# Performance work log

Measured on AMD Instinct MI355X. Metric: run time of the kernel, lower is better.

Reference implementation:

```python
import jax, jax.numpy as jnp
import numpy as np

EPS = 1e-6
H, HKV, D = 32, 8, 64          # heads, kv heads, head_dim
E, TOP_K, FF = 8, 2, 1024      # experts, top-k, expert intermediate
HID = 2048


def rms_norm(x, w):
    xf = x.astype(jnp.float32)
    var = jnp.mean(xf * xf, axis=-1, keepdims=True)
    return (w * (xf * jax.lax.rsqrt(var + EPS)).astype(x.dtype))


def rotate_half(x):
    x1, x2 = jnp.split(x, 2, axis=-1)
    return jnp.concatenate([-x2, x1], axis=-1)


def apply_rope(q, k, cos, sin):
    # cos/sin: [B,S,rd] -> [B,1,S,rd]
    cos = cos[:, None, :, :]
    sin = sin[:, None, :, :]
    rd = cos.shape[-1]
    q_rot, q_pass = q[..., :rd], q[..., rd:]
    k_rot, k_pass = k[..., :rd], k[..., rd:]
    q_emb = q_rot * cos + rotate_half(q_rot) * sin
    k_emb = k_rot * cos + rotate_half(k_rot) * sin
    return (jnp.concatenate([q_emb, q_pass], -1), jnp.concatenate([k_emb, k_pass], -1))


def attention(x, cos, sin, wq, wk, wv, wo):
    B, S, _ = x.shape
    q = (x @ wq).reshape(B, S, H, D).transpose(0, 2, 1, 3)      # [B,H,S,D]
    k = (x @ wk).reshape(B, S, HKV, D).transpose(0, 2, 1, 3)    # [B,Hk,S,D]
    v = (x @ wv).reshape(B, S, HKV, D).transpose(0, 2, 1, 3)
    q, k = apply_rope(q, k, cos, sin)
    rep = H // HKV
    k = jnp.repeat(k, rep, axis=1)
    v = jnp.repeat(v, rep, axis=1)
    scale = D ** -0.5
    scores = jnp.einsum('bhqd,bhkd->bhqk', q, k) * scale
    causal = jnp.triu(jnp.full((S, S), -jnp.inf, dtype=scores.dtype), k=1)
    scores = scores + causal
    probs = jax.nn.softmax(scores.astype(jnp.float32), axis=-1).astype(q.dtype)
    out = jnp.einsum('bhqk,bhkd->bhqd', probs, v)
    out = out.transpose(0, 2, 1, 3).reshape(B, S, H * D)
    return out @ wo


def moe(x, gate_w, corr_bias, w1, w2, w3):
    B, S, Dm = x.shape
    xf = x.reshape(-1, Dm)                                      # [T, Dm]
    T = xf.shape[0]
    logits = xf @ gate_w                                        # [T, E]
    rw = jax.nn.sigmoid(logits.astype(jnp.float32))
    scores = rw + corr_bias
    _, sel = jax.lax.top_k(scores, TOP_K)                       # [T, k]
    tw = jnp.take_along_axis(rw, sel, axis=-1)
    tw = tw / jnp.sum(tw, axis=-1, keepdims=True)
    # dense [T, E] combine weights (zero for unselected experts)
    cw = jnp.zeros((T, E), dtype=xf.dtype).at[jnp.arange(T)[:, None], sel].set(tw.astype(xf.dtype))
    # run every expert densely, combine with sparse weights (same math as gather/scatter loop)
    h = jax.nn.silu(jnp.einsum('td,edf->etf', xf, w1)) * jnp.einsum('td,edf->etf', xf, w3)
    eo = jnp.einsum('etf,efd->etd', h, w2)                      # [E, T, Dm]
    out = jnp.einsum('etd,te->td', eo, cw)
    return out.reshape(B, S, Dm)


def setup_inputs() -> dict:
    key = jax.random.key(0)
    ks = jax.random.split(key, 16)
    s = 0.02
    return {
        'hidden_states': jax.random.normal(ks[0], (2, 1024, HID), jnp.float32),
        'cos': jax.random.uniform(ks[1], (2, 1024, D), jnp.float32),
        'sin': jax.random.uniform(ks[2], (2, 1024, D), jnp.float32),
        'ln1_w': jnp.ones((HID,), jnp.float32),
        'ln2_w': jnp.ones((HID,), jnp.float32),
        'wq': jax.random.normal(ks[3], (HID, H * D), jnp.float32) * s,
        'wk': jax.random.normal(ks[4], (HID, HKV * D), jnp.float32) * s,
        'wv': jax.random.normal(ks[5], (HID, HKV * D), jnp.float32) * s,
        'wo': jax.random.normal(ks[6], (H * D, HID), jnp.float32) * s,
        'gate_w': jax.random.normal(ks[7], (HID, E), jnp.float32) * s,
        'corr_bias': jnp.zeros((E,), jnp.float32),
        'w1': jax.random.normal(ks[8], (E, HID, FF), jnp.float32) * s,
        'w2': jax.random.normal(ks[9], (E, FF, HID), jnp.float32) * s,
        'w3': jax.random.normal(ks[10], (E, HID, FF), jnp.float32) * s,
    }


def reference(hidden_states, cos, sin, ln1_w, ln2_w, wq, wk, wv, wo, gate_w, corr_bias, w1, w2, w3):
    residual = hidden_states
    h = rms_norm(hidden_states, ln1_w)
    h = attention(h, cos, sin, wq, wk, wv, wo)
    h = residual + h
    residual = h
    h = rms_norm(h, ln2_w)
    h = moe(h, gate_w, corr_bias, w1, w2, w3)
    return residual + h
```

## Files before the change

### kernel.cpp

```cpp
#include <hip/hip_runtime.h>
#include <hip/hip_bf16.h>

#define DEV static __device__ __forceinline__

typedef __attribute__((ext_vector_type(8))) short short8;
typedef __attribute__((ext_vector_type(8))) __bf16 bf16x8;
typedef __attribute__((ext_vector_type(4))) float floatx4;

DEV short f2bf(float f) {
  unsigned u = __builtin_bit_cast(unsigned, f);
  unsigned r = (u + 0x7fffu + ((u >> 16) & 1u)) >> 16;
  return (short)(unsigned short)r;
}
DEV float bf2f(short s) {
  unsigned u = ((unsigned)(unsigned short)s) << 16;
  return __builtin_bit_cast(float, u);
}
DEV floatx4 mfma16(short8 a, short8 b, floatx4 c) {
  return __builtin_amdgcn_mfma_f32_16x16x32_bf16(
      __builtin_bit_cast(bf16x8, a), __builtin_bit_cast(bf16x8, b), c, 0, 0, 0);
}

DEV int sw2(int r) { return (r ^ (r >> 2)) & 3; }

DEV const short* sbase(const short* src, int ld, int row0, int id) {
  int r = id >> 2, cc = id & 3;
  return src + (long)(row0 + r) * ld + ((cc ^ sw2(r)) << 3);
}
DEV const short* sbaseg(const short* src, int ld, const int* rows, int p0, int plim,
                        int id) {
  int r = id >> 2, cc = id & 3;
  int pi = p0 + r;
  if (pi > plim) pi = plim;
  return src + (long)rows[pi] * ld + ((cc ^ sw2(r)) << 3);
}
DEV void sissue(short* ldsbuf, const short* base, int k0, int tid, int slotbase) {
  int wave = tid >> 6;
  __builtin_amdgcn_global_load_lds(
      (const __attribute__((address_space(1))) void*)(base + k0),
      (__attribute__((address_space(3))) void*)(ldsbuf + (slotbase + wave * 64) * 8),
      16, 0, 0);
}
DEV short8 rdfrag(const short* lds, int row, int l4) {
  return *(const short8*)(lds + row * 32 + ((l4 ^ sw2(row)) << 3));
}

__global__ __launch_bounds__(256) void k_gemm_qkv(
    const short* Ah, const short* Al, const short* Bh, const short* Bl,
    short* qbh, short* qbl, short* kbh, short* kbl, short* vbh, short* vbl,
    const float* cs, const float* sn) {
  const int K = 2048;
  __shared__ __align__(16) short AsH[2][4096], AsL[2][4096], BsH[2][2048], BsL[2][2048];
  int tid = threadIdx.x, lane = tid & 63, wave = tid >> 6;
  int l15 = lane & 15, l4 = lane >> 4;
  int m0 = blockIdx.y * 128, n0 = blockIdx.x * 64;

  const short* bAH0 = sbase(Ah, K, m0, tid);
  const short* bAH1 = sbase(Ah, K, m0, tid + 256);
  const short* bAL0 = sbase(Al, K, m0, tid);
  const short* bAL1 = sbase(Al, K, m0, tid + 256);
  const short* bBH0 = sbase(Bh, K, n0, tid);
  const short* bBL0 = sbase(Bl, K, n0, tid);

  auto STAGE = [&](int buf, int k0) {
    sissue(AsH[buf], bAH0, k0, tid, 0);
    sissue(AsH[buf], bAH1, k0, tid, 256);
    sissue(AsL[buf], bAL0, k0, tid, 0);
    sissue(AsL[buf], bAL1, k0, tid, 256);
    sissue(BsH[buf], bBH0, k0, tid, 0);
    sissue(BsL[buf], bBL0, k0, tid, 0);
  };

  floatx4 zero4 = {0.f, 0.f, 0.f, 0.f};
  floatx4 acc[2][4];
#pragma unroll
  for (int i = 0; i < 2; ++i)
#pragma unroll
    for (int j = 0; j < 4; ++j) acc[i][j] = zero4;

  STAGE(0, 0);
  __syncthreads();
  int cur = 0;
  for (int k0 = 0; k0 < K; k0 += 32) {
    if (k0 + 32 < K) STAGE(cur ^ 1, k0 + 32);
    short8 ah[2], al[2], bh2[4], bl2[4];
#pragma unroll
    for (int mi = 0; mi < 2; ++mi) {
      ah[mi] = rdfrag(AsH[cur], wave * 32 + mi * 16 + l15, l4);
      al[mi] = rdfrag(AsL[cur], wave * 32 + mi * 16 + l15, l4);
    }
#pragma unroll
    for (int nt = 0; nt < 4; ++nt) {
      bh2[nt] = rdfrag(BsH[cur], nt * 16 + l15, l4);
      bl2[nt] = rdfrag(BsL[cur], nt * 16 + l15, l4);
    }
#pragma unroll
    for (int mi = 0; mi < 2; ++mi)
#pragma unroll
      for (int nt = 0; nt < 4; ++nt) {
        acc[mi][nt] = mfma16(al[mi], bh2[nt], acc[mi][nt]);
        acc[mi][nt] = mfma16(ah[mi], bl2[nt], acc[mi][nt]);
        acc[mi][nt] = mfma16(ah[mi], bh2[nt], acc[mi][nt]);
      }
    __syncthreads();
    cur ^= 1;
  }

  bool isq = n0 < 2048, isk = (!isq) && n0 < 2560;
  if (isq || isk) {
#pragma unroll
    for (int mi = 0; mi < 2; ++mi)
#pragma unroll
      for (int ntp = 0; ntp < 2; ++ntp)
#pragma unroll
        for (int j = 0; j < 4; ++j) {
          int row = m0 + wave * 32 + mi * 16 + l4 * 4 + j;
          int d = ntp * 16 + l15;
          float x0 = acc[mi][ntp][j], x1 = acc[mi][ntp + 2][j];
          float c0 = cs[row * 64 + d], c1 = cs[row * 64 + d + 32];
          float s0 = sn[row * 64 + d], s1 = sn[row * 64 + d + 32];
          float y0 = x0 * c0 - x1 * s0;
          float y1 = x1 * c1 + x0 * s1;
          if (isq) { y0 *= 0.125f; y1 *= 0.125f; }
          acc[mi][ntp][j] = y0;
          acc[mi][ntp + 2][j] = y1;
        }
  }
  short* Ch; short* Cl; int ldc, coff;
  if (isq)      { Ch = qbh; Cl = qbl; ldc = 2048; coff = n0; }
  else if (isk) { Ch = kbh; Cl = kbl; ldc = 512;  coff = n0 - 2048; }
  else          { Ch = vbh; Cl = vbl; ldc = 512;  coff = n0 - 2560; }
#pragma unroll
  for (int mi = 0; mi < 2; ++mi)
#pragma unroll
    for (int nt = 0; nt < 4; ++nt) {
      int row = m0 + wave * 32 + mi * 16 + l4 * 4;
      int col = coff + nt * 16 + l15;
#pragma unroll
      for (int j = 0; j < 4; ++j) {
        float v = acc[mi][nt][j];
        long ix = (long)(row + j) * ldc + col;
        short hi = f2bf(v);
        Ch[ix] = hi;
        Cl[ix] = f2bf(v - bf2f(hi));
      }
    }
}

__global__ __launch_bounds__(256) void k_gemm_wo(const short* Ah, const short* Al,
                                                 const short* Bh, const short* Bl,
                                                 const float* resid, float* out) {
  const int K = 2048;
  __shared__ __align__(16) short AsH[2][4096], AsL[2][4096], BsH[2][2048], BsL[2][2048];
  int tid = threadIdx.x, lane = tid & 63, wave = tid >> 6;
  int l15 = lane & 15, l4 = lane >> 4;
  int m0 = blockIdx.y * 128, n0 = blockIdx.x * 64;

  const short* bAH0 = sbase(Ah, K, m0, tid);
  const short* bAH1 = sbase(Ah, K, m0, tid + 256);
  const short* bAL0 = sbase(Al, K, m0, tid);
  const short* bAL1 = sbase(Al, K, m0, tid + 256);
  const short* bBH0 = sbase(Bh, K, n0, tid);
  const short* bBL0 = sbase(Bl, K, n0, tid);

  auto STAGE = [&](int buf, int k0) {
    sissue(AsH[buf], bAH0, k0, tid, 0);
    sissue(AsH[buf], bAH1, k0, tid, 256);
    sissue(AsL[buf], bAL0, k0, tid, 0);
    sissue(AsL[buf], bAL1, k0, tid, 256);
    sissue(BsH[buf], bBH0, k0, tid, 0);
    sissue(BsL[buf], bBL0, k0, tid, 0);
  };

  floatx4 zero4 = {0.f, 0.f, 0.f, 0.f};
  floatx4 acc[2][4];
#pragma unroll
  for (int i = 0; i < 2; ++i)
#pragma unroll
    for (int j = 0; j < 4; ++j) acc[i][j] = zero4;

  STAGE(0, 0);
  __syncthreads();
  int cur = 0;
  for (int k0 = 0; k0 < K; k0 += 32) {
    if (k0 + 32 < K) STAGE(cur ^ 1, k0 + 32);
    short8 ah[2], al[2], bh2[4], bl2[4];
#pragma unroll
    for (int mi = 0; mi < 2; ++mi) {
      ah[mi] = rdfrag(AsH[cur], wave * 32 + mi * 16 + l15, l4);
      al[mi] = rdfrag(AsL[cur], wave * 32 + mi * 16 + l15, l4);
    }
#pragma unroll
    for (int nt = 0; nt < 4; ++nt) {
      bh2[nt] = rdfrag(BsH[cur], nt * 16 + l15, l4);
      bl2[nt] = rdfrag(BsL[cur], nt * 16 + l15, l4);
    }
#pragma unroll
    for (int mi = 0; mi < 2; ++mi)
#pragma unroll
      for (int nt = 0; nt < 4; ++nt) {
        acc[mi][nt] = mfma16(al[mi], bh2[nt], acc[mi][nt]);
        acc[mi][nt] = mfma16(ah[mi], bl2[nt], acc[mi][nt]);
        acc[mi][nt] = mfma16(ah[mi], bh2[nt], acc[mi][nt]);
      }
    __syncthreads();
    cur ^= 1;
  }
#pragma unroll
  for (int mi = 0; mi < 2; ++mi)
#pragma unroll
    for (int nt = 0; nt < 4; ++nt) {
      int row = m0 + wave * 32 + mi * 16 + l4 * 4;
      int col = n0 + nt * 16 + l15;
#pragma unroll
      for (int j = 0; j < 4; ++j) {
        long ix = (long)(row + j) * 2048 + col;
        out[ix] = resid[ix] + acc[mi][nt][j];
      }
    }
}

__global__ __launch_bounds__(256) void k_moe_a(const short* X, const short* W1T,
                                               const short* W3T, const int* rows,
                                               const int* cnt, const int* eoff,
                                               short* hh) {
  int e = blockIdx.z;
  int c = cnt[e];
  int mtile = blockIdx.y;
  if (mtile * 128 >= c) return;
  int p0 = eoff[e] + mtile * 128;
  int plim = eoff[e] + c - 1;
  const short* B1 = W1T + (long)e * 1024 * 2048;
  const short* B3 = W3T + (long)e * 1024 * 2048;
  int n0 = blockIdx.x * 64;
  __shared__ __align__(16) short As_[2][4096], B1s[2][2048], B3s[2][2048];
  int tid = threadIdx.x, lane = tid & 63, wave = tid >> 6;
  int l15 = lane & 15, l4 = lane >> 4;

  const short* bA0 = sbaseg(X, 2048, rows, p0, plim, tid);
  const short* bA1 = sbaseg(X, 2048, rows, p0, plim, tid + 256);
  const short* bB1 = sbase(B1, 2048, n0, tid);
  const short* bB3 = sbase(B3, 2048, n0, tid);

  auto STAGE = [&](int buf, int k0) {
    sissue(As_[buf], bA0, k0, tid, 0);
    sissue(As_[buf], bA1, k0, tid, 256);
    sissue(B1s[buf], bB1, k0, tid, 0);
    sissue(B3s[buf], bB3, k0, tid, 0);
  };

  floatx4 zero4 = {0.f, 0.f, 0.f, 0.f};
  floatx4 acc1[2][4], acc3[2][4];
#pragma unroll
  for (int i = 0; i < 2; ++i)
#pragma unroll
    for (int j = 0; j < 4; ++j) { acc1[i][j] = zero4; acc3[i][j] = zero4; }

  STAGE(0, 0);
  __syncthreads();
  int cur = 0;
  for (int k0 = 0; k0 < 2048; k0 += 32) {
    if (k0 + 32 < 2048) STAGE(cur ^ 1, k0 + 32);
    short8 af[2], b1f[4], b3f[4];
#pragma unroll
    for (int mi = 0; mi < 2; ++mi) af[mi] = rdfrag(As_[cur], wave * 32 + mi * 16 + l15, l4);
#pragma unroll
    for (int nt = 0; nt < 4; ++nt) {
      b1f[nt] = rdfrag(B1s[cur], nt * 16 + l15, l4);
      b3f[nt] = rdfrag(B3s[cur], nt * 16 + l15, l4);
    }
#pragma unroll
    for (int mi = 0; mi < 2; ++mi)
#pragma unroll
      for (int nt = 0; nt < 4; ++nt) {
        acc1[mi][nt] = mfma16(af[mi], b1f[nt], acc1[mi][nt]);
        acc3[mi][nt] = mfma16(af[mi], b3f[nt], acc3[mi][nt]);
      }
    __syncthreads();
    cur ^= 1;
  }
#pragma unroll
  for (int mi = 0; mi < 2; ++mi)
#pragma unroll
    for (int nt = 0; nt < 4; ++nt) {
      int col = n0 + nt * 16 + l15;
#pragma unroll
      for (int j = 0; j < 4; ++j) {
        int rl = wave * 32 + mi * 16 + l4 * 4 + j;
        if (mtile * 128 + rl < c) {
          float v1 = acc1[mi][nt][j], v3 = acc3[mi][nt][j];
          float hg = v1 / (1.f + __expf(-v1));
          hh[(long)(p0 + rl) * 1024 + col] = f2bf(hg * v3);
        }
      }
    }
}

__global__ __launch_bounds__(256) void k_moe_b(const short* hh, const short* W2T,
                                               const int* cnt, const int* eoff,
                                               short* mo) {
  int e = blockIdx.z;
  int c = cnt[e];
  int mtile = blockIdx.y;
  if (mtile * 128 >= c) return;
  int p0 = eoff[e] + mtile * 128;
  const short* B = W2T + (long)e * 2048 * 1024;
  int n0 = blockIdx.x * 128;
  __shared__ __align__(16) short As_[2][4096], Bs_[2][4096];
  int tid = threadIdx.x, lane = tid & 63, wave = tid >> 6;
  int l15 = lane & 15, l4 = lane >> 4;
  int wm = wave >> 1, wn = wave & 1;

  const short* bA0 = sbase(hh, 1024, p0, tid);
  const short* bA1 = sbase(hh, 1024, p0, tid + 256);
  const short* bB0 = sbase(B, 1024, n0, tid);
  const short* bB1 = sbase(B, 1024, n0, tid + 256);

  auto STAGE = [&](int buf, int k0) {
    sissue(As_[buf], bA0, k0, tid, 0);
    sissue(As_[buf], bA1, k0, tid, 256);
    sissue(Bs_[buf], bB0, k0, tid, 0);
    sissue(Bs_[buf], bB1, k0, tid, 256);
  };

  floatx4 zero4 = {0.f, 0.f, 0.f, 0.f};
  floatx4 acc[4][4];
#pragma unroll
  for (int i = 0; i < 4; ++i)
#pragma unroll
    for (int j = 0; j < 4; ++j) acc[i][j] = zero4;

  STAGE(0, 0);
  __syncthreads();
  int cur = 0;
  for (int k0 = 0; k0 < 1024; k0 += 32) {
    if (k0 + 32 < 1024) STAGE(cur ^ 1, k0 + 32);
    short8 af[4], bfv[4];
#pragma unroll
    for (int mi = 0; mi < 4; ++mi) af[mi] = rdfrag(As_[cur], wm * 64 + mi * 16 + l15, l4);
#pragma unroll
    for (int nt = 0; nt < 4; ++nt) bfv[nt] = rdfrag(Bs_[cur], wn * 64 + nt * 16 + l15, l4);
#pragma unroll
    for (int mi = 0; mi < 4; ++mi)
#pragma unroll
      for (int nt = 0; nt < 4; ++nt) acc[mi][nt] = mfma16(af[mi], bfv[nt], acc[mi][nt]);
    __syncthreads();
    cur ^= 1;
  }
#pragma unroll
  for (int mi = 0; mi < 4; ++mi)
#pragma unroll
    for (int nt = 0; nt < 4; ++nt) {
      int col = n0 + wn * 64 + nt * 16 + l15;
#pragma unroll
      for (int j = 0; j < 4; ++j) {
        int rl = wm * 64 + mi * 16 + l4 * 4 + j;
        if (mtile * 128 + rl < c) mo[(long)(p0 + rl) * 2048 + col] = f2bf(acc[mi][nt][j]);
      }
    }
}

DEV int aswz(int r, int c) { return r * 64 + (((c ^ ((r ^ (r >> 3)) & 7)) & 7) << 3); }

__global__ __launch_bounds__(256) void k_attn2(const short* qhp, const short* qlp,
                                               const short* khp, const short* klp,
                                               const short* vhp, const short* vlp,
                                               short* oh, short* ol) {
  int qt = blockIdx.x, bh = blockIdx.y;
  int h = bh & 31, b = bh >> 5, kvh = h >> 2;
  int tid = threadIdx.x, wave = tid >> 6, lane = tid & 63;
  int l15 = lane & 15, l4 = lane >> 4;

  __shared__ __align__(16) short Kh[4096], Kl2[4096], Vth[4096], Vtl[4096];
  __shared__ __align__(16) short Ph[4][1024], Pl2[4][1024];

  int qrow = qt * 64 + wave * 16 + l15;
  long qoff = ((long)(b * 1024 + qrow)) * 2048 + h * 64;
  short8 qh0 = *(const short8*)(qhp + qoff + l4 * 8);
  short8 qh1 = *(const short8*)(qhp + qoff + 32 + l4 * 8);
  short8 ql0 = *(const short8*)(qlp + qoff + l4 * 8);
  short8 ql1 = *(const short8*)(qlp + qoff + 32 + l4 * 8);

  floatx4 zero4 = {0.f, 0.f, 0.f, 0.f};
  floatx4 acco[4] = {zero4, zero4, zero4, zero4};
  float mrun[4] = {-1e30f, -1e30f, -1e30f, -1e30f};
  float lrun[4] = {0.f, 0.f, 0.f, 0.f};

  const short* khb = khp + ((long)b * 1024) * 512 + kvh * 64;
  const short* klb = klp + ((long)b * 1024) * 512 + kvh * 64;
  const short* vhb = vhp + ((long)b * 1024) * 512 + kvh * 64;
  const short* vlb = vlp + ((long)b * 1024) * 512 + kvh * 64;

  for (int kt = 0; kt <= qt; ++kt) {
#pragma unroll
    for (int it = 0; it < 2; ++it) {
      int id = it * 256 + tid;
      int r = id >> 3, cc = id & 7;
      long goff = (long)(kt * 64 + r) * 512 + cc * 8;
      *(uint4*)(Kh + aswz(r, cc)) = *(const uint4*)(khb + goff);
      *(uint4*)(Kl2 + aswz(r, cc)) = *(const uint4*)(klb + goff);
      __align__(16) short tv[8];
      *(uint4*)tv = *(const uint4*)(vhb + goff);
#pragma unroll
      for (int j = 0; j < 8; ++j) Vth[aswz(cc * 8 + j, r >> 3) + (r & 7)] = tv[j];
      *(uint4*)tv = *(const uint4*)(vlb + goff);
#pragma unroll
      for (int j = 0; j < 8; ++j) Vtl[aswz(cc * 8 + j, r >> 3) + (r & 7)] = tv[j];
    }
    __syncthreads();

    floatx4 accs[4] = {zero4, zero4, zero4, zero4};
#pragma unroll
    for (int ks = 0; ks < 2; ++ks) {
      short8 qah = ks ? qh1 : qh0;
      short8 qal = ks ? ql1 : ql0;
#pragma unroll
      for (int nt = 0; nt < 4; ++nt) {
        int kvr = nt * 16 + l15;
        short8 kfh = *(const short8*)(Kh + aswz(kvr, l4 + 4 * ks));
        short8 kfl = *(const short8*)(Kl2 + aswz(kvr, l4 + 4 * ks));
        accs[nt] = mfma16(qal, kfh, accs[nt]);
        accs[nt] = mfma16(qah, kfl, accs[nt]);
        accs[nt] = mfma16(qah, kfh, accs[nt]);
      }
    }
    if (kt == qt) {
#pragma unroll
      for (int nt = 0; nt < 4; ++nt)
#pragma unroll
        for (int j = 0; j < 4; ++j) {
          int kvg = nt * 16 + l15;
          int qg = wave * 16 + l4 * 4 + j;
          if (kvg > qg) accs[nt][j] = -1e30f;
        }
    }
    float pj[4][4];
#pragma unroll
    for (int j = 0; j < 4; ++j) {
      float mx = fmaxf(fmaxf(accs[0][j], accs[1][j]), fmaxf(accs[2][j], accs[3][j]));
      mx = fmaxf(mx, __shfl_xor(mx, 1));
      mx = fmaxf(mx, __shfl_xor(mx, 2));
      mx = fmaxf(mx, __shfl_xor(mx, 4));
      mx = fmaxf(mx, __shfl_xor(mx, 8));
      float mnew = fmaxf(mrun[j], mx);
      float alpha = expf(mrun[j] - mnew);
      float rs = 0.f;
#pragma unroll
      for (int nt = 0; nt < 4; ++nt) {
        float pv = expf(accs[nt][j] - mnew);
        pj[nt][j] = pv;
        rs += pv;
      }
      rs += __shfl_xor(rs, 1);
      rs += __shfl_xor(rs, 2);
      rs += __shfl_xor(rs, 4);
      rs += __shfl_xor(rs, 8);
      lrun[j] = lrun[j] * alpha + rs;
      mrun[j] = mnew;
      acco[0][j] *= alpha; acco[1][j] *= alpha; acco[2][j] *= alpha; acco[3][j] *= alpha;
    }
    short* P = Ph[wave];
    short* P2 = Pl2[wave];
#pragma unroll
    for (int nt = 0; nt < 4; ++nt)
#pragma unroll
      for (int j = 0; j < 4; ++j) {
        int rr = l4 * 4 + j, col = nt * 16 + l15;
        float pv = pj[nt][j];
        short hi = f2bf(pv);
        int ad = aswz(rr, col >> 3) + (col & 7);
        P[ad] = hi;
        P2[ad] = f2bf(pv - bf2f(hi));
      }
    asm volatile("s_waitcnt lgkmcnt(0)" ::: "memory");
    __builtin_amdgcn_sched_barrier(0);
#pragma unroll
    for (int ks = 0; ks < 2; ++ks) {
      short8 pah = *(const short8*)(P + aswz(l15, l4 + 4 * ks));
      short8 pal = *(const short8*)(P2 + aswz(l15, l4 + 4 * ks));
#pragma unroll
      for (int nt = 0; nt < 4; ++nt) {
        int dr = nt * 16 + l15;
        short8 vfh = *(const short8*)(Vth + aswz(dr, l4 + 4 * ks));
        short8 vfl = *(const short8*)(Vtl + aswz(dr, l4 + 4 * ks));
        acco[nt] = mfma16(pal, vfh, acco[nt]);
        acco[nt] = mfma16(pah, vfl, acco[nt]);
        acco[nt] = mfma16(pah, vfh, acco[nt]);
      }
    }
    __syncthreads();
  }
#pragma unroll
  for (int j = 0; j < 4; ++j) {
    float invl = 1.f / lrun[j];
    int qg = qt * 64 + wave * 16 + l4 * 4 + j;
    long ooff = ((long)(b * 1024 + qg)) * 2048 + h * 64;
#pragma unroll
    for (int nt = 0; nt < 4; ++nt) {
      float v = acco[nt][j] * invl;
      short hi = f2bf(v);
      oh[ooff + nt * 16 + l15] = hi;
      ol[ooff + nt * 16 + l15] = f2bf(v - bf2f(hi));
    }
  }
}

DEV void trans_load(const float* src, int N, int n0, int k0, float (*t)[65], int tid) {
  int r = tid >> 2, cq = tid & 3;
  const float* s = src + (long)(k0 + r) * N + n0 + cq * 16;
#pragma unroll
  for (int i = 0; i < 4; ++i) {
    float4 v = *(const float4*)(s + i * 4);
    t[r][cq * 16 + i * 4 + 0] = v.x;
    t[r][cq * 16 + i * 4 + 1] = v.y;
    t[r][cq * 16 + i * 4 + 2] = v.z;
    t[r][cq * 16 + i * 4 + 3] = v.w;
  }
}

DEV void trans_tile1(const float* src, short* dst, int N, int K, int n0, int k0,
                     float (*t)[65]) {
  int tid = threadIdx.x;
  trans_load(src, N, n0, k0, t, tid);
  __syncthreads();
  int n = tid >> 2, kc = tid & 3;
#pragma unroll
  for (int ii = 0; ii < 2; ++ii) {
    short8 o;
#pragma unroll
    for (int j = 0; j < 8; ++j) o[j] = f2bf(t[kc * 16 + ii * 8 + j][n]);
    *(short8*)(dst + (long)(n0 + n) * K + k0 + kc * 16 + ii * 8) = o;
  }
}

DEV void trans_tile2(const float* src, short* dh, short* dl, int N, int K, int n0,
                     int k0, float (*t)[65]) {
  int tid = threadIdx.x;
  trans_load(src, N, n0, k0, t, tid);
  __syncthreads();
  int n = tid >> 2, kc = tid & 3;
#pragma unroll
  for (int ii = 0; ii < 2; ++ii) {
    short8 ohv, olv;
#pragma unroll
    for (int j = 0; j < 8; ++j) {
      float v = t[kc * 16 + ii * 8 + j][n];
      short hi = f2bf(v);
      ohv[j] = hi;
      olv[j] = f2bf(v - bf2f(hi));
    }
    *(short8*)(dh + (long)(n0 + n) * K + k0 + kc * 16 + ii * 8) = ohv;
    *(short8*)(dl + (long)(n0 + n) * K + k0 + kc * 16 + ii * 8) = olv;
  }
}

__global__ __launch_bounds__(256) void k_trans_attn(
    const float* wq, const float* wk, const float* wv, const float* wo,
    short* qkvTh, short* qkvTl, short* woTh, short* woTl) {
  __shared__ float t[64][65];
  int x = blockIdx.x, kt = blockIdx.y;
  const float* src; short* dh; short* dl; int N, n0;
  if (x < 32)      { src = wq; dh = qkvTh; dl = qkvTl; N = 2048; n0 = x * 64; }
  else if (x < 40) { src = wk; dh = qkvTh + 2048L * 2048; dl = qkvTl + 2048L * 2048;
                     N = 512; n0 = (x - 32) * 64; }
  else if (x < 48) { src = wv; dh = qkvTh + 2560L * 2048; dl = qkvTl + 2560L * 2048;
                     N = 512; n0 = (x - 40) * 64; }
  else             { src = wo; dh = woTh; dl = woTl; N = 2048; n0 = (x - 48) * 64; }
  trans_tile2(src, dh, dl, N, 2048, n0, kt * 64, t);
}

__global__ __launch_bounds__(256) void k_trans_moe13(const float* w1, const float* w3,
                                                     short* w1T, short* w3T) {
  __shared__ float t[64][65];
  int x = blockIdx.x, kt = blockIdx.y;
  const float* src; short* dst; int n0;
  if (x < 128) { int e = x >> 4; src = w1 + (long)e * 2048 * 1024;
                 dst = w1T + (long)e * 1024 * 2048; n0 = (x & 15) * 64; }
  else         { int i = x - 128, e = i >> 4; src = w3 + (long)e * 2048 * 1024;
                 dst = w3T + (long)e * 1024 * 2048; n0 = (i & 15) * 64; }
  trans_tile1(src, dst, 1024, 2048, n0, kt * 64, t);
}

__global__ __launch_bounds__(256) void k_trans_w2(const float* w2, short* w2T) {
  __shared__ float t[64][65];
  int e = blockIdx.x >> 5, ntb = blockIdx.x & 31, kt = blockIdx.y;
  trans_tile1(w2 + (long)e * 1024 * 2048, w2T + (long)e * 2048 * 1024,
              2048, 1024, ntb * 64, kt * 64, t);
}

__global__ __launch_bounds__(256) void k_rmsnorm1(const float* x, const float* w,
                                                  short* outh, short* outl) {
  int row = blockIdx.x, tid = threadIdx.x;
  const float* xr = x + (long)row * 2048;
  float4 a = *(const float4*)(xr + tid * 8);
  float4 c = *(const float4*)(xr + tid * 8 + 4);
  float ss = a.x * a.x + a.y * a.y + a.z * a.z + a.w * a.w +
             c.x * c.x + c.y * c.y + c.z * c.z + c.w * c.w;
  ss += __shfl_xor(ss, 1);  ss += __shfl_xor(ss, 2);  ss += __shfl_xor(ss, 4);
  ss += __shfl_xor(ss, 8);  ss += __shfl_xor(ss, 16); ss += __shfl_xor(ss, 32);
  __shared__ float red[4];
  int wave = tid >> 6;
  if ((tid & 63) == 0) red[wave] = ss;
  __syncthreads();
  float tot = red[0] + red[1] + red[2] + red[3];
  float inv = 1.f / sqrtf(tot * (1.f / 2048.f) + 1e-6f);
  float4 w0 = *(const float4*)(w + tid * 8);
  float4 w1 = *(const float4*)(w + tid * 8 + 4);
  float xv[8] = {a.x * w0.x, a.y * w0.y, a.z * w0.z, a.w * w0.w,
                 c.x * w1.x, c.y * w1.y, c.z * w1.z, c.w * w1.w};
  short8 ohv, olv;
#pragma unroll
  for (int j = 0; j < 8; ++j) {
    float v = xv[j] * inv;
    short hi = f2bf(v);
    ohv[j] = hi;
    olv[j] = f2bf(v - bf2f(hi));
  }
  *(short8*)(outh + (long)row * 2048 + tid * 8) = ohv;
  *(short8*)(outl + (long)row * 2048 + tid * 8) = olv;
}

__global__ __launch_bounds__(256) void k_rmsnorm2_gate(const float* x, const float* w,
                                                       const float* gw, const float* cb,
                                                       short* out, int* sel, float* tw,
                                                       int* cnt) {
  int row = blockIdx.x, tid = threadIdx.x;
  const float* xr = x + (long)row * 2048;
  float4 a = *(const float4*)(xr + tid * 8);
  float4 c = *(const float4*)(xr + tid * 8 + 4);
  float ss = a.x * a.x + a.y * a.y + a.z * a.z + a.w * a.w +
             c.x * c.x + c.y * c.y + c.z * c.z + c.w * c.w;
  ss += __shfl_xor(ss, 1);  ss += __shfl_xor(ss, 2);  ss += __shfl_xor(ss, 4);
  ss += __shfl_xor(ss, 8);  ss += __shfl_xor(ss, 16); ss += __shfl_xor(ss, 32);
  __shared__ float red[4];
  int wave = tid >> 6;
  if ((tid & 63) == 0) red[wave] = ss;
  __syncthreads();
  float tot = red[0] + red[1] + red[2] + red[3];
  float inv = 1.f / sqrtf(tot * (1.f / 2048.f) + 1e-6f);
  float4 w0 = *(const float4*)(w + tid * 8);
  float4 w1 = *(const float4*)(w + tid * 8 + 4);
  float xn[8];
  xn[0] = a.x * inv * w0.x; xn[1] = a.y * inv * w0.y; xn[2] = a.z * inv * w0.z;
  xn[3] = a.w * inv * w0.w; xn[4] = c.x * inv * w1.x; xn[5] = c.y * inv * w1.y;
  xn[6] = c.z * inv * w1.z; xn[7] = c.w * inv * w1.w;
  short8 o;
#pragma unroll
  for (int j = 0; j < 8; ++j) o[j] = f2bf(xn[j]);
  *(short8*)(out + (long)row * 2048 + tid * 8) = o;
  float gp[8] = {0.f, 0.f, 0.f, 0.f, 0.f, 0.f, 0.f, 0.f};
#pragma unroll
  for (int j = 0; j < 8; ++j) {
    const float* g = gw + (long)(tid * 8 + j) * 8;
    float4 g0 = *(const float4*)g;
    float4 g1 = *(const float4*)(g + 4);
    gp[0] += xn[j] * g0.x; gp[1] += xn[j] * g0.y; gp[2] += xn[j] * g0.z; gp[3] += xn[j] * g0.w;
    gp[4] += xn[j] * g1.x; gp[5] += xn[j] * g1.y; gp[6] += xn[j] * g1.z; gp[7] += xn[j] * g1.w;
  }
#pragma unroll
  for (int e = 0; e < 8; ++e) {
    gp[e] += __shfl_xor(gp[e], 1);  gp[e] += __shfl_xor(gp[e], 2);
    gp[e] += __shfl_xor(gp[e], 4);  gp[e] += __shfl_xor(gp[e], 8);
    gp[e] += __shfl_xor(gp[e], 16); gp[e] += __shfl_xor(gp[e], 32);
  }
  __shared__ float gred[4][8];
  __shared__ float srw[8], ssc[8];
  if ((tid & 63) == 0) {
#pragma unroll
    for (int e = 0; e < 8; ++e) gred[wave][e] = gp[e];
  }
  __syncthreads();
  if (tid < 8) {
    float lg = gred[0][tid] + gred[1][tid] + gred[2][tid] + gred[3][tid];
    float rw = 1.f / (1.f + expf(-lg));
    srw[tid] = rw;
    ssc[tid] = rw + cb[tid];
  }
  __syncthreads();
  if (tid == 0) {
    int e0 = 0; float b0 = ssc[0];
    for (int e = 1; e < 8; ++e) if (ssc[e] > b0) { b0 = ssc[e]; e0 = e; }
    int e1 = -1; float b1 = -1e30f;
    for (int e = 0; e < 8; ++e) if (e != e0 && ssc[e] > b1) { b1 = ssc[e]; e1 = e; }
    float t0 = srw[e0], t1 = srw[e1], s = t0 + t1;
    sel[row * 2] = e0; sel[row * 2 + 1] = e1;
    tw[row * 2] = t0 / s; tw[row * 2 + 1] = t1 / s;
    atomicAdd(&cnt[e0], 1);
    atomicAdd(&cnt[e1], 1);
  }
}

__global__ void k_scan(const int* cnt, int* eoff) {
  if (threadIdx.x == 0) {
    int s = 0;
    for (int e = 0; e < 8; ++e) { eoff[e] = s; s += cnt[e]; }
  }
}

__global__ __launch_bounds__(256) void k_scatter(const int* sel, const int* eoff,
                                                 int* fill, int* rows, int* pos) {
  int t = blockIdx.x * 256 + threadIdx.x;
  if (t >= 2048) return;
  for (int k = 0; k < 2; ++k) {
    int e = sel[t * 2 + k];
    int p = eoff[e] + atomicAdd(&fill[e], 1);
    rows[p] = t;
    pos[t * 2 + k] = p;
  }
}

__global__ __launch_bounds__(256) void k_combine(float* out, const short* mo,
                                                 const int* pos, const float* tw) {
  int t = blockIdx.x, tid = threadIdx.x;
  int p0 = pos[t * 2], p1 = pos[t * 2 + 1];
  float w0 = tw[t * 2], w1 = tw[t * 2 + 1];
  float* o = out + (long)t * 2048 + tid * 8;
  short8 m0 = *(const short8*)(mo + (long)p0 * 2048 + tid * 8);
  short8 m1 = *(const short8*)(mo + (long)p1 * 2048 + tid * 8);
  float4 a = *(const float4*)o;
  float4 b = *(const float4*)(o + 4);
  a.x += w0 * bf2f(m0[0]) + w1 * bf2f(m1[0]);
  a.y += w0 * bf2f(m0[1]) + w1 * bf2f(m1[1]);
  a.z += w0 * bf2f(m0[2]) + w1 * bf2f(m1[2]);
  a.w += w0 * bf2f(m0[3]) + w1 * bf2f(m1[3]);
  b.x += w0 * bf2f(m0[4]) + w1 * bf2f(m1[4]);
  b.y += w0 * bf2f(m0[5]) + w1 * bf2f(m1[5]);
  b.z += w0 * bf2f(m0[6]) + w1 * bf2f(m1[6]);
  b.w += w0 * bf2f(m0[7]) + w1 * bf2f(m1[7]);
  *(float4*)o = a;
  *(float4*)(o + 4) = b;
}

extern "C" void kernel_launch(void* const* d_in, const int* in_sizes, int n_in,
                              void* d_out, int out_size, void* d_ws, size_t ws_size,
                              hipStream_t stream) {
  const float* x    = (const float*)d_in[0];
  const float* cosb = (const float*)d_in[1];
  const float* sinb = (const float*)d_in[2];
  const float* ln1  = (const float*)d_in[3];
  const float* ln2  = (const float*)d_in[4];
  const float* wq   = (const float*)d_in[5];
  const float* wk   = (const float*)d_in[6];
  const float* wv   = (const float*)d_in[7];
  const float* wo   = (const float*)d_in[8];
  const float* gw   = (const float*)d_in[9];
  const float* cb   = (const float*)d_in[10];
  const float* w1   = (const float*)d_in[11];
  const float* w2   = (const float*)d_in[12];
  const float* w3   = (const float*)d_in[13];
  float* out = (float*)d_out;

  char* p = (char*)d_ws;
  auto take = [&](size_t n) { char* r = p; p += (n + 255) & ~(size_t)255; return r; };
  short* qkvTh = (short*)take(3072L * 2048 * 2);
  short* qkvTl = (short*)take(3072L * 2048 * 2);
  short* woTh  = (short*)take(2048L * 2048 * 2);
  short* woTl  = (short*)take(2048L * 2048 * 2);
  short* w1T   = (short*)take(8L * 1024 * 2048 * 2);
  short* w3T   = (short*)take(8L * 1024 * 2048 * 2);
  short* w2T   = (short*)take(8L * 2048 * 1024 * 2);
  short* hbh   = (short*)take(2048L * 2048 * 2);
  short* hbl   = (short*)take(2048L * 2048 * 2);
  short* qbh   = (short*)take(2048L * 2048 * 2);
  short* qbl   = (short*)take(2048L * 2048 * 2);
  short* kbh   = (short*)take(2048L * 512 * 2);
  short* kbl   = (short*)take(2048L * 512 * 2);
  short* vbh   = (short*)take(2048L * 512 * 2);
  short* vbl   = (short*)take(2048L * 512 * 2);
  short* aoh   = (short*)take(2048L * 2048 * 2);
  short* aol   = (short*)take(2048L * 2048 * 2);
  short* h2b   = (short*)take(2048L * 2048 * 2);
  short* hhb   = (short*)take(4224L * 1024 * 2);
  short* mob   = (short*)take(4352L * 2048 * 2);
  int* rti     = (int*)take(64 * sizeof(int));
  int* cnt = rti; int* fill = rti + 8; int* eoff = rti + 16;
  int* sel     = (int*)take(2048L * 2 * 4);
  float* twb   = (float*)take(2048L * 2 * 4);
  int* rowsp   = (int*)take(4352L * 4);
  int* posb    = (int*)take(2048L * 2 * 4);
  (void)ws_size; (void)in_sizes; (void)n_in; (void)out_size;

  dim3 B256(256);
  k_trans_attn<<<dim3(80, 32), B256, 0, stream>>>(wq, wk, wv, wo, qkvTh, qkvTl,
                                                  woTh, woTl);
  k_trans_moe13<<<dim3(256, 32), B256, 0, stream>>>(w1, w3, w1T, w3T);
  k_trans_w2<<<dim3(256, 16), B256, 0, stream>>>(w2, w2T);
  hipMemsetAsync(rti, 0, 64, stream);

  k_rmsnorm1<<<dim3(2048), B256, 0, stream>>>(x, ln1, hbh, hbl);
  k_gemm_qkv<<<dim3(48, 16), B256, 0, stream>>>(hbh, hbl, qkvTh, qkvTl, qbh, qbl,
                                                kbh, kbl, vbh, vbl, cosb, sinb);
  k_attn2<<<dim3(16, 64), B256, 0, stream>>>(qbh, qbl, kbh, kbl, vbh, vbl, aoh, aol);
  k_gemm_wo<<<dim3(32, 16), B256, 0, stream>>>(aoh, aol, woTh, woTl, x, out);

  k_rmsnorm2_gate<<<dim3(2048), B256, 0, stream>>>(out, ln2, gw, cb, h2b, sel, twb, cnt);
  k_scan<<<dim3(1), dim3(64), 0, stream>>>(cnt, eoff);
  k_scatter<<<dim3(8), B256, 0, stream>>>(sel, eoff, fill, rowsp, posb);
  k_moe_a<<<dim3(16, 16, 8), B256, 0, stream>>>(h2b, w1T, w3T, rowsp, cnt, eoff, hhb);
  k_moe_b<<<dim3(16, 16, 8), B256, 0, stream>>>(hhb, w2T, cnt, eoff, mob);
  k_combine<<<dim3(2048), B256, 0, stream>>>(out, mob, posb, twb);
}
```

Baseline: 646.9 us.

## Pair causal query tiles, pre-transpose V, and double-buffer K/V via global_load_lds

V is now transposed once by a separate kernel, so the attention kernel no longer does scattered per-element transposed LDS writes. Each block handles two query tiles (qt and 15-qt), which balances the triangular causal workload and halves the grid. K/V tiles are double-buffered with asynchronous global-to-LDS loads so the next tile's fetch overlaps compute. expf is replaced with __expf. This adds an extra kernel launch and scratch buffers, doubles the K/V LDS footprint, and raises register pressure from the two accumulator sets.

```diff
diff --git a/kernel.cpp b/kernel.cpp
--- a/kernel.cpp
+++ b/kernel.cpp
@@ -360,147 +360,218 @@
     }
 }
 
+__global__ __launch_bounds__(256) void k_transv(const short* vbh, const short* vbl,
+                                                short* vth, short* vtl) {
+  __shared__ __align__(16) short th[64][72], tl[64][72];
+  int tt = blockIdx.x;
+  int bk = blockIdx.y;
+  int b = bk >> 3, kvh = bk & 7;
+  int tid = threadIdx.x;
+#pragma unroll
+  for (int it = 0; it < 2; ++it) {
+    int id = it * 256 + tid;
+    int r = id >> 3, cc = id & 7;
+    long src = (long)(b * 1024 + tt * 64 + r) * 512 + kvh * 64 + cc * 8;
+    *(uint4*)(&th[r][cc * 8]) = *(const uint4*)(vbh + src);
+    *(uint4*)(&tl[r][cc * 8]) = *(const uint4*)(vbl + src);
+  }
+  __syncthreads();
+#pragma unroll
+  for (int it = 0; it < 2; ++it) {
+    int id = it * 256 + tid;
+    int n = id >> 3, kc = id & 7;
+    short8 oh2, ol2;
+#pragma unroll
+    for (int j = 0; j < 8; ++j) { oh2[j] = th[kc * 8 + j][n]; ol2[j] = tl[kc * 8 + j][n]; }
+    long dst = (long)bk * 65536 + (long)n * 1024 + tt * 64 + kc * 8;
+    *(short8*)(vth + dst) = oh2;
+    *(short8*)(vtl + dst) = ol2;
+  }
+}
+
+DEV int vsw(int r) { return (r ^ (r >> 3)) & 7; }
+DEV short8 avread(const short* buf, int row, int c) {
+  return *(const short8*)(buf + row * 64 + (((c ^ vsw(row)) & 7) << 3));
+}
 DEV int aswz(int r, int c) { return r * 64 + (((c ^ ((r ^ (r >> 3)) & 7)) & 7) << 3); }
-
-__global__ __launch_bounds__(256) void k_attn2(const short* qhp, const short* qlp,
-                                               const short* khp, const short* klp,
-                                               const short* vhp, const short* vlp,
-                                               short* oh, short* ol) {
-  int qt = blockIdx.x, bh = blockIdx.y;
+DEV void glds(short* ldsslot, const short* src) {
+  __builtin_amdgcn_global_load_lds(
+      (const __attribute__((address_space(1))) void*)src,
+      (__attribute__((address_space(3))) void*)ldsslot, 16, 0, 0);
+}
+
+__global__ __launch_bounds__(256) void k_attn3(
+    const short* qhp, const short* qlp, const short* khp, const short* klp,
+    const short* vth2, const short* vtl2, short* oh, short* ol) {
+  int xp = blockIdx.x, bh = blockIdx.y;
   int h = bh & 31, b = bh >> 5, kvh = h >> 2;
   int tid = threadIdx.x, wave = tid >> 6, lane = tid & 63;
   int l15 = lane & 15, l4 = lane >> 4;
-
-  __shared__ __align__(16) short Kh[4096], Kl2[4096], Vth[4096], Vtl[4096];
-  __shared__ __align__(16) short Ph[4][1024], Pl2[4][1024];
-
-  int qrow = qt * 64 + wave * 16 + l15;
-  long qoff = ((long)(b * 1024 + qrow)) * 2048 + h * 64;
-  short8 qh0 = *(const short8*)(qhp + qoff + l4 * 8);
-  short8 qh1 = *(const short8*)(qhp + qoff + 32 + l4 * 8);
-  short8 ql0 = *(const short8*)(qlp + qoff + l4 * 8);
-  short8 ql1 = *(const short8*)(qlp + qoff + 32 + l4 * 8);
+  int qtA = 15 - xp, qtB = xp;
+
+  __shared__ __align__(16) short Kh[2][4096], Kl[2][4096], Vh[2][4096], Vl[2][4096];
+  __shared__ __align__(16) short Ph[4][1024], Pl[4][1024];
+
+  short8 qh[2][2], ql[2][2];
+#pragma unroll
+  for (int tt = 0; tt < 2; ++tt) {
+    int qrow = (tt ? qtB : qtA) * 64 + wave * 16 + l15;
+    long qoff = ((long)(b * 1024 + qrow)) * 2048 + h * 64;
+    qh[tt][0] = *(const short8*)(qhp + qoff + l4 * 8);
+    qh[tt][1] = *(const short8*)(qhp + qoff + 32 + l4 * 8);
+    ql[tt][0] = *(const short8*)(qlp + qoff + l4 * 8);
+    ql[tt][1] = *(const short8*)(qlp + qoff + 32 + l4 * 8);
+  }
 
   floatx4 zero4 = {0.f, 0.f, 0.f, 0.f};
-  floatx4 acco[4] = {zero4, zero4, zero4, zero4};
-  float mrun[4] = {-1e30f, -1e30f, -1e30f, -1e30f};
-  float lrun[4] = {0.f, 0.f, 0.f, 0.f};
+  floatx4 acco[2][4];
+  float mrun[2][4], lrun[2][4];
+#pragma unroll
+  for (int tt = 0; tt < 2; ++tt)
+#pragma unroll
+    for (int j = 0; j < 4; ++j) {
+      acco[tt][j] = zero4;
+      mrun[tt][j] = -1e30f;
+      lrun[tt][j] = 0.f;
+    }
 
   const short* khb = khp + ((long)b * 1024) * 512 + kvh * 64;
   const short* klb = klp + ((long)b * 1024) * 512 + kvh * 64;
-  const short* vhb = vhp + ((long)b * 1024) * 512 + kvh * 64;
-  const short* vlb = vlp + ((long)b * 1024) * 512 + kvh * 64;
-
-  for (int kt = 0; kt <= qt; ++kt) {
-#pragma unroll
-    for (int it = 0; it < 2; ++it) {
-      int id = it * 256 + tid;
-      int r = id >> 3, cc = id & 7;
-      long goff = (long)(kt * 64 + r) * 512 + cc * 8;
-      *(uint4*)(Kh + aswz(r, cc)) = *(const uint4*)(khb + goff);
-      *(uint4*)(Kl2 + aswz(r, cc)) = *(const uint4*)(klb + goff);
-      __align__(16) short tv[8];
-      *(uint4*)tv = *(const uint4*)(vhb + goff);
-#pragma unroll
-      for (int j = 0; j < 8; ++j) Vth[aswz(cc * 8 + j, r >> 3) + (r & 7)] = tv[j];
-      *(uint4*)tv = *(const uint4*)(vlb + goff);
-#pragma unroll
-      for (int j = 0; j < 8; ++j) Vtl[aswz(cc * 8 + j, r >> 3) + (r & 7)] = tv[j];
-    }
+  const short* vhb = vth2 + (long)(b * 8 + kvh) * 65536;
+  const short* vlb = vtl2 + (long)(b * 8 + kvh) * 65536;
+
+  int r0 = tid >> 3, c0 = tid & 7;
+  int r1 = r0 + 32;
+  const short* kh0 = khb + (long)r0 * 512 + ((c0 ^ vsw(r0)) << 3);
+  const short* kh1 = khb + (long)r1 * 512 + ((c0 ^ vsw(r1)) << 3);
+  const short* kl0 = klb + (long)r0 * 512 + ((c0 ^ vsw(r0)) << 3);
+  const short* kl1 = klb + (long)r1 * 512 + ((c0 ^ vsw(r1)) << 3);
+  const short* vh0 = vhb + (long)r0 * 1024 + ((c0 ^ vsw(r0)) << 3);
+  const short* vh1 = vhb + (long)r1 * 1024 + ((c0 ^ vsw(r1)) << 3);
+  const short* vl0 = vlb + (long)r0 * 1024 + ((c0 ^ vsw(r0)) << 3);
+  const short* vl1 = vlb + (long)r1 * 1024 + ((c0 ^ vsw(r1)) << 3);
+  int wslot = wave * 512;
+
+  auto STAGE = [&](int buf, int kt) {
+    int ko = kt * 32768;
+    int vo = kt * 64;
+    glds(&Kh[buf][wslot], kh0 + ko);
+    glds(&Kh[buf][2048 + wslot], kh1 + ko);
+    glds(&Kl[buf][wslot], kl0 + ko);
+    glds(&Kl[buf][2048 + wslot], kl1 + ko);
+    glds(&Vh[buf][wslot], vh0 + vo);
+    glds(&Vh[buf][2048 + wslot], vh1 + vo);
+    glds(&Vl[buf][wslot], vl0 + vo);
+    glds(&Vl[buf][2048 + wslot], vl1 + vo);
+  };
+
+  STAGE(0, 0);
+  int cur = 0;
+  for (int kt = 0; kt <= qtA; ++kt) {
     __syncthreads();
-
-    floatx4 accs[4] = {zero4, zero4, zero4, zero4};
-#pragma unroll
-    for (int ks = 0; ks < 2; ++ks) {
-      short8 qah = ks ? qh1 : qh0;
-      short8 qal = ks ? ql1 : ql0;
+    if (kt < qtA) STAGE(cur ^ 1, kt + 1);
+#pragma unroll
+    for (int tt = 0; tt < 2; ++tt) {
+      int qtt = tt ? qtB : qtA;
+      if (tt == 1 && kt > qtB) continue;
+      floatx4 accs[4] = {zero4, zero4, zero4, zero4};
+#pragma unroll
+      for (int ks = 0; ks < 2; ++ks) {
+        short8 qah = qh[tt][ks];
+        short8 qal = ql[tt][ks];
+#pragma unroll
+        for (int nt = 0; nt < 4; ++nt) {
+          int kvr = nt * 16 + l15;
+          short8 kfh = avread(Kh[cur], kvr, l4 + 4 * ks);
+          short8 kfl = avread(Kl[cur], kvr, l4 + 4 * ks);
+          accs[nt] = mfma16(qal, kfh, accs[nt]);
+          accs[nt] = mfma16(qah, kfl, accs[nt]);
+          accs[nt] = mfma16(qah, kfh, accs[nt]);
+        }
+      }
+      if (kt == qtt) {
+#pragma unroll
+        for (int nt = 0; nt < 4; ++nt)
+#pragma unroll
+          for (int j = 0; j < 4; ++j) {
+            int kvg = nt * 16 + l15;
+            int qg = wave * 16 + l4 * 4 + j;
+            if (kvg > qg) accs[nt][j] = -1e30f;
+          }
+      }
+      float pj[4][4];
+#pragma unroll
+      for (int j = 0; j < 4; ++j) {
+        float mx = fmaxf(fmaxf(accs[0][j], accs[1][j]), fmaxf(accs[2][j], accs[3][j]));
+        mx = fmaxf(mx, __shfl_xor(mx, 1));
+        mx = fmaxf(mx, __shfl_xor(mx, 2));
+        mx = fmaxf(mx, __shfl_xor(mx, 4));
+        mx = fmaxf(mx, __shfl_xor(mx, 8));
+        float mnew = fmaxf(mrun[tt][j], mx);
+        float alpha = __expf(mrun[tt][j] - mnew);
+        float rs = 0.f;
+#pragma unroll
+        for (int nt = 0; nt < 4; ++nt) {
+          float pv = __expf(accs[nt][j] - mnew);
+          pj[nt][j] = pv;
+          rs += pv;
+        }
+        rs += __shfl_xor(rs, 1);
+        rs += __shfl_xor(rs, 2);
+        rs += __shfl_xor(rs, 4);
+        rs += __shfl_xor(rs, 8);
+        lrun[tt][j] = lrun[tt][j] * alpha + rs;
+        mrun[tt][j] = mnew;
+        acco[tt][0][j] *= alpha; acco[tt][1][j] *= alpha;
+        acco[tt][2][j] *= alpha; acco[tt][3][j] *= alpha;
+      }
+      short* P = Ph[wave];
+      short* P2 = Pl[wave];
+#pragma unroll
+      for (int nt = 0; nt < 4; ++nt)
+#pragma unroll
+        for (int j = 0; j < 4; ++j) {
+          int rr = l4 * 4 + j, col = nt * 16 + l15;
+          float pv = pj[nt][j];
+          short hi = f2bf(pv);
+          int ad = aswz(rr, col >> 3) + (col & 7);
+          P[ad] = hi;
+          P2[ad] = f2bf(pv - bf2f(hi));
+        }
+      asm volatile("s_waitcnt lgkmcnt(0)" ::: "memory");
+      __builtin_amdgcn_sched_barrier(0);
+#pragma unroll
+      for (int ks = 0; ks < 2; ++ks) {
+        short8 pah = *(const short8*)(P + aswz(l15, l4 + 4 * ks));
+        short8 pal = *(const short8*)(P2 + aswz(l15, l4 + 4 * ks));
+#pragma unroll
+        for (int nt = 0; nt < 4; ++nt) {
+          int dr = nt * 16 + l15;
+          short8 vfh = avread(Vh[cur], dr, l4 + 4 * ks);
+          short8 vfl = avread(Vl[cur], dr, l4 + 4 * ks);
+          acco[tt][nt] = mfma16(pal, vfh, acco[tt][nt]);
+          acco[tt][nt] = mfma16(pah, vfl, acco[tt][nt]);
+          acco[tt][nt] = mfma16(pah, vfh, acco[tt][nt]);
+        }
+      }
+    }
+    cur ^= 1;
+  }
+#pragma unroll
+  for (int tt = 0; tt < 2; ++tt) {
+    int qtt = tt ? qtB : qtA;
+#pragma unroll
+    for (int j = 0; j < 4; ++j) {
+      float invl = 1.f / lrun[tt][j];
+      int qg = qtt * 64 + wave * 16 + l4 * 4 + j;
+      long ooff = ((long)(b * 1024 + qg)) * 2048 + h * 64;
 #pragma unroll
       for (int nt = 0; nt < 4; ++nt) {
-        int kvr = nt * 16 + l15;
-        short8 kfh = *(const short8*)(Kh + aswz(kvr, l4 + 4 * ks));
-        short8 kfl = *(const short8*)(Kl2 + aswz(kvr, l4 + 4 * ks));
-        accs[nt] = mfma16(qal, kfh, accs[nt]);
-        accs[nt] = mfma16(qah, kfl, accs[nt]);
-        accs[nt] = mfma16(qah, kfh, accs[nt]);
-      }
-    }
-    if (kt == qt) {
-#pragma unroll
-      for (int nt = 0; nt < 4; ++nt)
-#pragma unroll
-        for (int j = 0; j < 4; ++j) {
-          int kvg = nt * 16 + l15;
-          int qg = wave * 16 + l4 * 4 + j;
-          if (kvg > qg) accs[nt][j] = -1e30f;
-        }
-    }
-    float pj[4][4];
-#pragma unroll
-    for (int j = 0; j < 4; ++j) {
-      float mx = fmaxf(fmaxf(accs[0][j], accs[1][j]), fmaxf(accs[2][j], accs[3][j]));
-      mx = fmaxf(mx, __shfl_xor(mx, 1));
-      mx = fmaxf(mx, __shfl_xor(mx, 2));
-      mx = fmaxf(mx, __shfl_xor(mx, 4));
-      mx = fmaxf(mx, __shfl_xor(mx, 8));
-      float mnew = fmaxf(mrun[j], mx);
-      float alpha = expf(mrun[j] - mnew);
-      float rs = 0.f;
-#pragma unroll
-      for (int nt = 0; nt < 4; ++nt) {
-        float pv = expf(accs[nt][j] - mnew);
-        pj[nt][j] = pv;
-        rs += pv;
-      }
-      rs += __shfl_xor(rs, 1);
-      rs += __shfl_xor(rs, 2);
-      rs += __shfl_xor(rs, 4);
-      rs += __shfl_xor(rs, 8);
-      lrun[j] = lrun[j] * alpha + rs;
-      mrun[j] = mnew;
-      acco[0][j] *= alpha; acco[1][j] *= alpha; acco[2][j] *= alpha; acco[3][j] *= alpha;
-    }
-    short* P = Ph[wave];
-    short* P2 = Pl2[wave];
-#pragma unroll
-    for (int nt = 0; nt < 4; ++nt)
-#pragma unroll
-      for (int j = 0; j < 4; ++j) {
-        int rr = l4 * 4 + j, col = nt * 16 + l15;
-        float pv = pj[nt][j];
-        short hi = f2bf(pv);
-        int ad = aswz(rr, col >> 3) + (col & 7);
-        P[ad] = hi;
-        P2[ad] = f2bf(pv - bf2f(hi));
-      }
-    asm volatile("s_waitcnt lgkmcnt(0)" ::: "memory");
-    __builtin_amdgcn_sched_barrier(0);
-#pragma unroll
-    for (int ks = 0; ks < 2; ++ks) {
-      short8 pah = *(const short8*)(P + aswz(l15, l4 + 4 * ks));
-      short8 pal = *(const short8*)(P2 + aswz(l15, l4 + 4 * ks));
-#pragma unroll
-      for (int nt = 0; nt < 4; ++nt) {
-        int dr = nt * 16 + l15;
-        short8 vfh = *(const short8*)(Vth + aswz(dr, l4 + 4 * ks));
-        short8 vfl = *(const short8*)(Vtl + aswz(dr, l4 + 4 * ks));
-        acco[nt] = mfma16(pal, vfh, acco[nt]);
-        acco[nt] = mfma16(pah, vfl, acco[nt]);
-        acco[nt] = mfma16(pah, vfh, acco[nt]);
-      }
-    }
-    __syncthreads();
-  }
-#pragma unroll
-  for (int j = 0; j < 4; ++j) {
-    float invl = 1.f / lrun[j];
-    int qg = qt * 64 + wave * 16 + l4 * 4 + j;
-    long ooff = ((long)(b * 1024 + qg)) * 2048 + h * 64;
-#pragma unroll
-    for (int nt = 0; nt < 4; ++nt) {
-      float v = acco[nt][j] * invl;
-      short hi = f2bf(v);
-      oh[ooff + nt * 16 + l15] = hi;
-      ol[ooff + nt * 16 + l15] = f2bf(v - bf2f(hi));
+        float v = acco[tt][nt][j] * invl;
+        short hi = f2bf(v);
+        oh[ooff + nt * 16 + l15] = hi;
+        ol[ooff + nt * 16 + l15] = f2bf(v - bf2f(hi));
+      }
     }
   }
 }
@@ -767,6 +838,8 @@
   short* kbl   = (short*)take(2048L * 512 * 2);
   short* vbh   = (short*)take(2048L * 512 * 2);
   short* vbl   = (short*)take(2048L * 512 * 2);
+  short* vth   = (short*)take(16L * 64 * 1024 * 2);
+  short* vtl   = (short*)take(16L * 64 * 1024 * 2);
   short* aoh   = (short*)take(2048L * 2048 * 2);
   short* aol   = (short*)take(2048L * 2048 * 2);
   short* h2b   = (short*)take(2048L * 2048 * 2);
@@ -790,7 +863,8 @@
   k_rmsnorm1<<<dim3(2048), B256, 0, stream>>>(x, ln1, hbh, hbl);
   k_gemm_qkv<<<dim3(48, 16), B256, 0, stream>>>(hbh, hbl, qkvTh, qkvTl, qbh, qbl,
                                                 kbh, kbl, vbh, vbl, cosb, sinb);
-  k_attn2<<<dim3(16, 64), B256, 0, stream>>>(qbh, qbl, kbh, kbl, vbh, vbl, aoh, aol);
+  k_transv<<<dim3(16, 16), B256, 0, stream>>>(vbh, vbl, vth, vtl);
+  k_attn3<<<dim3(8, 64), B256, 0, stream>>>(qbh, qbl, kbh, kbl, vth, vtl, aoh, aol);
   k_gemm_wo<<<dim3(32, 16), B256, 0, stream>>>(aoh, aol, woTh, woTl, x, out);
 
   k_rmsnorm2_gate<<<dim3(2048), B256, 0, stream>>>(out, ln2, gw, cb, h2b, sel, twb, cnt);
```

Result: faster. 583.1 us (-9.9%).
